# Optimization experiments

Measured on AMD Instinct MI355X. Metric: run time of the kernel, lower is better.

## Reference

```python
import jax, jax.numpy as jnp
import numpy as np

BETA = 0.25  # init kwarg; exercises the 0 <= beta < 1 loss branch


def setup_inputs() -> dict:
    key = jax.random.key(0)
    k1, k2 = jax.random.split(key)
    N, D, K = 65536, 64, 4096
    x = jax.random.normal(k1, (N, D), dtype=jnp.float32)
    # original: uniform(-1/K, 1/K) then mean-centered; exact init distribution
    codebook = jax.random.uniform(k2, (K, D), dtype=jnp.float32,
                                  minval=-1.0 / K, maxval=1.0 / K)
    codebook = codebook - codebook.mean(axis=0, keepdims=True)
    return {"x": x, "codebook": codebook}


def reference(x, codebook):
    # pairwise squared distances via sum-of-squares + matmul: [N, K]
    dist = (jnp.sum(x * x, axis=1, keepdims=True)
            + jnp.sum(codebook * codebook, axis=1)
            - 2.0 * jnp.matmul(x, codebook.T))
    encoding_inds = jnp.argmin(dist, axis=1)            # [N]
    # gather codebook rows (equivalent to one-hot @ codebook, no one-hot materialized)
    quantized = jnp.take(codebook, encoding_inds, axis=0)  # [N, D]
    # straight-through estimator
    x_quantized = x + jax.lax.stop_gradient(quantized - x)
    mse = lambda a, b: jnp.mean((a - b) ** 2)
    loss = (BETA * mse(x, jax.lax.stop_gradient(quantized))
            + mse(quantized, jax.lax.stop_gradient(x)))
    return x_quantized, encoding_inds[:, None], loss
```

## Files before the change

kernel.cpp:

```cpp
#include <hip/hip_runtime.h>


#define D  64
#define NT 256
#define PH 128

typedef unsigned short u16;
typedef short bf16x8 __attribute__((ext_vector_type(8)));
typedef float f32x4  __attribute__((ext_vector_type(4)));

#define VMWAIT(n) asm volatile("s_waitcnt vmcnt(" #n ")" ::: "memory")

__device__ __forceinline__ u16 f32_to_bf16_raw(float f) {
    union { float f; unsigned u; } v; v.f = f;
    unsigned u = v.u;
    u += 0x7FFFu + ((u >> 16) & 1u);
    return (u16)(u >> 16);
}
__device__ __forceinline__ float bf16_raw_to_f32(u16 h) {
    union { unsigned u; float f; } v; v.u = ((unsigned)h) << 16;
    return v.f;
}
__device__ __forceinline__ f32x4 mfma16(bf16x8 a, bf16x8 b, f32x4 c) {
    return __builtin_amdgcn_mfma_f32_16x16x32_bf16(a, b, c, 0, 0, 0);
}

__device__ __forceinline__ float np_pairwise_sumsq_64(const float* p) {
    float r[8];
    #pragma unroll
    for (int j = 0; j < 8; ++j) r[j] = __fmul_rn(p[j], p[j]);
    #pragma unroll
    for (int i = 8; i < 64; i += 8) {
        #pragma unroll
        for (int j = 0; j < 8; ++j)
            r[j] = __fadd_rn(r[j], __fmul_rn(p[i + j], p[i + j]));
    }
    float t0 = __fadd_rn(r[0], r[1]);
    float t1 = __fadd_rn(r[2], r[3]);
    float t2 = __fadd_rn(r[4], r[5]);
    float t3 = __fadd_rn(r[6], r[7]);
    return __fadd_rn(__fadd_rn(t0, t1), __fadd_rn(t2, t3));
}

__global__ __launch_bounds__(256) void rowsumsq_kernel(const float* __restrict__ a,
                                                       float* __restrict__ out, int nrows) {
    int r = blockIdx.x * 256 + threadIdx.x;
    if (r >= nrows) return;
    float buf[64];
    const float4* p = (const float4*)(a + (size_t)r * D);
    #pragma unroll
    for (int i = 0; i < 16; ++i) {
        float4 v = p[i];
        buf[4*i] = v.x; buf[4*i+1] = v.y; buf[4*i+2] = v.z; buf[4*i+3] = v.w;
    }
    out[r] = np_pairwise_sumsq_64(buf);
}

__global__ __launch_bounds__(256) void pack_cb2(const float* __restrict__ cb,
                                                bf16x8* __restrict__ cbf) {
    int t = blockIdx.x;
    int tid = threadIdx.x;
    int lane = tid & 63;
    int ks = (tid >> 6) & 1;
    int hl = tid >> 7;
    int code = t * 16 + (lane & 15);
    int g = lane >> 4;
    bf16x8 v;
    #pragma unroll
    for (int j = 0; j < 8; ++j) {
        int d = ks * 32 + g * 4 + (j & 3) + 16 * (j >> 2);
        float val = cb[(size_t)code * D + d];
        u16 h = f32_to_bf16_raw(val);
        if (hl) {
            float resid = val - bf16_raw_to_f32(h);
            h = f32_to_bf16_raw(resid);
        }
        v[j] = (short)h;
    }
    cbf[((size_t)t * 4 + hl * 2 + ks) * 64 + lane] = v;
}

#define MARG_A 8.0e-6f
#define MARG_B 5.0e-7f

__global__ __launch_bounds__(256, 2) void phase1_kernel(
    const float* __restrict__ x, const float* __restrict__ sx,
    const float* __restrict__ sc, const bf16x8* __restrict__ cbf,
    int* __restrict__ idxbuf, int* __restrict__ amb_cnt, int* __restrict__ amb_rows)
{
    __shared__ __align__(16) char ring[4][8192];
    __shared__ float scl[4096];

    const int tid  = threadIdx.x;
    const int w    = tid >> 6;
    const int lane = tid & 63;
    const int r = lane & 15, g = lane >> 4;
    const int rowA = blockIdx.x * 128 + w * 32 + r;
    const int rowB = rowA + 16;

    for (int j = tid; j < 1024; j += 256)
        *(float4*)&scl[j * 4] = *(const float4*)&sc[j * 4];

    bf16x8 A0h, A1h, A0l, A1l, B0h, B1h, B0l, B1l;
    {
        const float* xr = x + (size_t)rowA * D;
        float e0[8], e1[8];
        float4 f0 = *(const float4*)(xr + g * 4);
        float4 f1 = *(const float4*)(xr + 16 + g * 4);
        float4 f2 = *(const float4*)(xr + 32 + g * 4);
        float4 f3 = *(const float4*)(xr + 48 + g * 4);
        e0[0]=f0.x;e0[1]=f0.y;e0[2]=f0.z;e0[3]=f0.w; e0[4]=f1.x;e0[5]=f1.y;e0[6]=f1.z;e0[7]=f1.w;
        e1[0]=f2.x;e1[1]=f2.y;e1[2]=f2.z;e1[3]=f2.w; e1[4]=f3.x;e1[5]=f3.y;e1[6]=f3.z;e1[7]=f3.w;
        #pragma unroll
        for (int j = 0; j < 8; ++j) {
            u16 h0 = f32_to_bf16_raw(e0[j]);
            A0h[j] = (short)h0; A0l[j] = (short)f32_to_bf16_raw(e0[j] - bf16_raw_to_f32(h0));
            u16 h1 = f32_to_bf16_raw(e1[j]);
            A1h[j] = (short)h1; A1l[j] = (short)f32_to_bf16_raw(e1[j] - bf16_raw_to_f32(h1));
        }
    }
    {
        const float* xr = x + (size_t)rowB * D;
        float e0[8], e1[8];
        float4 f0 = *(const float4*)(xr + g * 4);
        float4 f1 = *(const float4*)(xr + 16 + g * 4);
        float4 f2 = *(const float4*)(xr + 32 + g * 4);
        float4 f3 = *(const float4*)(xr + 48 + g * 4);
        e0[0]=f0.x;e0[1]=f0.y;e0[2]=f0.z;e0[3]=f0.w; e0[4]=f1.x;e0[5]=f1.y;e0[6]=f1.z;e0[7]=f1.w;
        e1[0]=f2.x;e1[1]=f2.y;e1[2]=f2.z;e1[3]=f2.w; e1[4]=f3.x;e1[5]=f3.y;e1[6]=f3.z;e1[7]=f3.w;
        #pragma unroll
        for (int j = 0; j < 8; ++j) {
            u16 h0 = f32_to_bf16_raw(e0[j]);
            B0h[j] = (short)h0; B0l[j] = (short)f32_to_bf16_raw(e0[j] - bf16_raw_to_f32(h0));
            u16 h1 = f32_to_bf16_raw(e1[j]);
            B1h[j] = (short)h1; B1l[j] = (short)f32_to_bf16_raw(e1[j] - bf16_raw_to_f32(h1));
        }
    }

    float sxr[8], m1[8], m2[8];
    int   i1[8];
    #pragma unroll
    for (int u = 0; u < 8; ++u) {
        int orow = blockIdx.x * 128 + w * 32 + (u >> 2) * 16 + g * 4 + (u & 3);
        sxr[u] = sx[orow];
        m1[u] = 3.4e38f; m2[u] = 3.4e38f; i1[u] = 0;
    }

    auto stage = [&](int p, int buf) {
        const char* src = (const char*)cbf + (size_t)p * 8192 + tid * 16;
        #pragma unroll
        for (int i = 0; i < 2; ++i) {
            __builtin_amdgcn_global_load_lds(
                (const __attribute__((address_space(1))) unsigned int*)(src + i * 4096),
                (__attribute__((address_space(3))) unsigned int*)&ring[buf][i * 4096 + w * 1024 + lane * 16],
                16, 0, 0);
        }
    };

    auto compute = [&](int p, int buf) {
        #pragma unroll
        for (int tt = 0; tt < 2; ++tt) {
            int t = 2 * p + tt;
            const bf16x8* bf = (const bf16x8*)&ring[buf][tt * 4096];
            bf16x8 b0h = bf[0 * 64 + lane];
            bf16x8 b1h = bf[1 * 64 + lane];
            bf16x8 b0l = bf[2 * 64 + lane];
            bf16x8 b1l = bf[3 * 64 + lane];

            f32x4 accA = {0.f, 0.f, 0.f, 0.f};
            f32x4 accB = {0.f, 0.f, 0.f, 0.f};
            accA = mfma16(A0h, b0h, accA);  accB = mfma16(B0h, b0h, accB);
            accA = mfma16(A1h, b1h, accA);  accB = mfma16(B1h, b1h, accB);
            accA = mfma16(A0h, b0l, accA);  accB = mfma16(B0h, b0l, accB);
            accA = mfma16(A1h, b1l, accA);  accB = mfma16(B1h, b1l, accB);
            accA = mfma16(A0l, b0h, accA);  accB = mfma16(B0l, b0h, accB);
            accA = mfma16(A1l, b1h, accA);  accB = mfma16(B1l, b1h, accB);

            float sck = scl[t * 16 + r];
            int   kc  = t * 16 + r;
            #pragma unroll
            for (int q = 0; q < 4; ++q) {
                float s = __fmaf_rn(-2.0f, accA[q], __fadd_rn(sxr[q], sck));
                m2[q] = fminf(m2[q], fmaxf(m1[q], s));
                bool lt = s < m1[q];
                i1[q] = lt ? kc : i1[q];
                m1[q] = fminf(m1[q], s);
            }
            #pragma unroll
            for (int q = 0; q < 4; ++q) {
                float s = __fmaf_rn(-2.0f, accB[q], __fadd_rn(sxr[4 + q], sck));
                m2[4+q] = fminf(m2[4+q], fmaxf(m1[4+q], s));
                bool lt = s < m1[4+q];
                i1[4+q] = lt ? kc : i1[4+q];
                m1[4+q] = fminf(m1[4+q], s);
            }
        }
    };

    VMWAIT(0);
    stage(0, 0); stage(1, 1); stage(2, 2);

    for (int p = 0; p < PH - 3; ++p) {
        VMWAIT(4);
        __syncthreads();
        stage(p + 3, (p + 3) & 3);
        compute(p, p & 3);
    }
    VMWAIT(4); __syncthreads(); compute(PH - 3, (PH - 3) & 3);
    VMWAIT(2); __syncthreads(); compute(PH - 2, (PH - 2) & 3);
    VMWAIT(0); __syncthreads(); compute(PH - 1, (PH - 1) & 3);

    #pragma unroll
    for (int u = 0; u < 8; ++u) {
        #pragma unroll
        for (int mm = 1; mm < 16; mm <<= 1) {
            float om1 = __shfl_xor(m1[u], mm, 64);
            float om2 = __shfl_xor(m2[u], mm, 64);
            int   oi1 = __shfl_xor(i1[u], mm, 64);
            float nm2 = fminf(fmaxf(m1[u], om1), fminf(m2[u], om2));
            i1[u] = (om1 < m1[u]) ? oi1 : i1[u];
            m1[u] = fminf(m1[u], om1);
            m2[u] = nm2;
        }
    }
    if (r == 0) {
        #pragma unroll
        for (int u = 0; u < 8; ++u) {
            int orow = blockIdx.x * 128 + w * 32 + (u >> 2) * 16 + g * 4 + (u & 3);
            idxbuf[orow] = i1[u];
            float marg = __fmaf_rn(sxr[u], MARG_B, MARG_A);
            if (m2[u] - m1[u] <= marg) {
                int slot = atomicAdd(amb_cnt, 1);
                amb_rows[slot] = orow;
            }
        }
    }
}

__global__ __launch_bounds__(256) void exact_scan(
    const float* __restrict__ x, const float* __restrict__ cb,
    const float* __restrict__ sx, const float* __restrict__ sc,
    const int* __restrict__ amb_cnt, const int* __restrict__ amb_rows,
    int* __restrict__ idxbuf)
{
    __shared__ float csT[4][64][64];
    __shared__ float xsT[64][16];
    __shared__ float redv[16][64];
    __shared__ int   redi[16][64];
    __shared__ float sxl[16];
    __shared__ int   rowids[16];

    const int tid = threadIdx.x;
    const int cnt = *amb_cnt;
    const int tz = tid >> 6, ty = (tid >> 4) & 3, cx = tid & 15;

    for (int base = blockIdx.x * 16; base < cnt; base += gridDim.x * 16) {
        if (tid < 16) {
            int i = base + tid;
            int rr = (i < cnt) ? amb_rows[i] : amb_rows[base];
            rowids[tid] = rr;
            sxl[tid] = sx[rr];
        }
        __syncthreads();
        {
            int rr = rowids[tid >> 4];
            int dg = tid & 15;
            float4 v = *(const float4*)(x + (size_t)rr * D + dg * 4);
            xsT[dg*4+0][tid>>4] = v.x; xsT[dg*4+1][tid>>4] = v.y;
            xsT[dg*4+2][tid>>4] = v.z; xsT[dg*4+3][tid>>4] = v.w;
        }

        float bv[4]; int bi[4];
        #pragma unroll
        for (int i = 0; i < 4; ++i) { bv[i] = 3.4e38f; bi[i] = 0x7fffffff; }

        for (int st = 0; st < 16; ++st) {
            __syncthreads();
            {
                int code = st * 256 + tid;
                const float4* src = (const float4*)(cb + (size_t)code * D);
                #pragma unroll
                for (int dd = 0; dd < 16; ++dd) {
                    float4 v = src[dd];
                    csT[tid>>6][dd*4+0][tid&63] = v.x; csT[tid>>6][dd*4+1][tid&63] = v.y;
                    csT[tid>>6][dd*4+2][tid&63] = v.z; csT[tid>>6][dd*4+3][tid&63] = v.w;
                }
            }
            __syncthreads();

            float acc[4][4];
            #pragma unroll
            for (int i = 0; i < 4; ++i)
                #pragma unroll
                for (int j = 0; j < 4; ++j) acc[i][j] = 0.0f;

            #pragma unroll 4
            for (int d = 0; d < 64; ++d) {
                float4 xv = *(const float4*)&xsT[d][ty * 4];
                float4 cv = *(const float4*)&csT[tz][d][cx * 4];
                float xr[4] = {xv.x, xv.y, xv.z, xv.w};
                float cc[4] = {cv.x, cv.y, cv.z, cv.w};
                #pragma unroll
                for (int i = 0; i < 4; ++i)
                    #pragma unroll
                    for (int j = 0; j < 4; ++j)
                        acc[i][j] = __fmaf_rn(xr[i], cc[j], acc[i][j]);
            }
            #pragma unroll
            for (int j = 0; j < 4; ++j) {
                int k = st * 256 + tz * 64 + cx * 4 + j;
                float sck = sc[k];
                #pragma unroll
                for (int i = 0; i < 4; ++i) {
                    float tt = __fadd_rn(sxl[ty * 4 + i], sck);
                    float u  = __fmul_rn(2.0f, acc[i][j]);
                    float s  = __fsub_rn(tt, u);
                    if (s < bv[i] || (s == bv[i] && k < bi[i])) { bv[i] = s; bi[i] = k; }
                }
            }
        }

        #pragma unroll
        for (int i = 0; i < 4; ++i) { redv[ty*4+i][tz*16+cx] = bv[i]; redi[ty*4+i][tz*16+cx] = bi[i]; }
        __syncthreads();
        if (tid < 16) {
            float bvv = redv[tid][0]; int bii = redi[tid][0];
            #pragma unroll 8
            for (int i = 1; i < 64; ++i) {
                float v = redv[tid][i]; int k = redi[tid][i];
                if (v < bvv || (v == bvv && k < bii)) { bvv = v; bii = k; }
            }
            idxbuf[rowids[tid]] = bii;
        }
        __syncthreads();
    }
}

__global__ __launch_bounds__(256) void finalize_rows(
    const float* __restrict__ x, const float* __restrict__ cb,
    const int* __restrict__ idxbuf,
    float* __restrict__ out_q, float* __restrict__ out_i,
    double* __restrict__ partials, int N)
{
    __shared__ double wsum[4];
    int wid = threadIdx.x >> 6, lane = threadIdx.x & 63;
    int n = blockIdx.x * 4 + wid;

    int idx = idxbuf[n];
    float q  = cb[(size_t)idx * D + lane];
    float xv = x[(size_t)n * D + lane];
    out_q[(size_t)n * D + lane] = q;

    double diff = (double)xv - (double)q;
    double s = diff * diff;
    #pragma unroll
    for (int off = 32; off > 0; off >>= 1) s += __shfl_down(s, off, 64);
    if (lane == 0) { wsum[wid] = s; out_i[n] = (float)idx; }
    __syncthreads();
    if (threadIdx.x == 0) partials[blockIdx.x] = (wsum[0] + wsum[1]) + (wsum[2] + wsum[3]);
}

__global__ __launch_bounds__(256) void loss_kernel(const double* __restrict__ partials,
                                                   int nP, float* __restrict__ out_loss,
                                                   double invND)
{
    __shared__ double red[256];
    double s = 0.0;
    for (int i = threadIdx.x; i < nP; i += 256) s += partials[i];
    red[threadIdx.x] = s;
    __syncthreads();
    #pragma unroll
    for (int step = 128; step > 0; step >>= 1) {
        if ((int)threadIdx.x < step) red[threadIdx.x] += red[threadIdx.x + step];
        __syncthreads();
    }
    if (threadIdx.x == 0) {
        double m = red[0] * invND;
        out_loss[0] = (float)(0.25 * m + m);
    }
}

extern "C" void kernel_launch(void* const* d_in, const int* in_sizes, int n_in,
                              void* d_out, int out_size, void* d_ws, size_t ws_size,
                              hipStream_t stream)
{
    const float* x  = (const float*)d_in[0];
    const float* cb = (const float*)d_in[1];
    const int N = in_sizes[0] / D;
    const int K = in_sizes[1] / D;

    float* out      = (float*)d_out;
    float* out_q    = out;
    float* out_i    = out + (size_t)N * D;
    float* out_loss = out_i + N;

    char* ws = (char*)d_ws;
    bf16x8* cbf      = (bf16x8*)ws;
    size_t off = (size_t)(K / 16) * 4 * 64 * sizeof(bf16x8);
    float*  sx       = (float*)(ws + off);  off += (size_t)N * 4;
    float*  sc       = (float*)(ws + off);  off += (size_t)K * 4;
    int*    idxbuf   = (int*)(ws + off);    off += (size_t)N * 4;
    int*    amb_rows = (int*)(ws + off);    off += (size_t)N * 4;
    double* partials = (double*)(ws + off); off += (size_t)(N / 4) * 8;
    int*    amb_cnt  = (int*)(ws + off);

    hipMemsetAsync(amb_cnt, 0, sizeof(int), stream);
    rowsumsq_kernel<<<(N + 255) / 256, 256, 0, stream>>>(x, sx, N);
    rowsumsq_kernel<<<(K + 255) / 256, 256, 0, stream>>>(cb, sc, K);
    pack_cb2<<<K / 16, 256, 0, stream>>>(cb, cbf);
    phase1_kernel<<<N / 128, 256, 0, stream>>>(x, sx, sc, cbf, idxbuf, amb_cnt, amb_rows);
    exact_scan<<<512, 256, 0, stream>>>(x, cb, sx, sc, amb_cnt, amb_rows, idxbuf);
    finalize_rows<<<N / 4, 256, 0, stream>>>(x, cb, idxbuf, out_q, out_i, partials, N);
    loss_kernel<<<1, 256, 0, stream>>>(partials, N / 4, out_loss,
                                       1.0 / ((double)N * (double)D));
}
```

Measured before the change: 303.1 us.

## Split codebook across wave pairs with per-wave rings and fuse prep kernels

Merges the memset, both row sum-of-squares kernels and the codebook packing into one prep kernel to cut launch overhead. In phase1 each wave now owns 64 rows and half of the codebook tiles, which doubles A-fragment reuse per loaded B tile and halves the LDS traffic per MFMA. Each wave also streams through its own 3-deep LDS ring without block-wide barriers, using setprio around the MFMA burst. The two halves' top-2 results are merged through shared memory at the end; in exchange register pressure rises (16 rows of state plus 4x A fragments), which could lower occupancy.

```diff
diff --git a/kernel.cpp b/kernel.cpp
--- a/kernel.cpp
+++ b/kernel.cpp
@@ -3,7 +3,6 @@
 
 #define D  64
 #define NT 256
-#define PH 128
 
 typedef unsigned short u16;
 typedef short bf16x8 __attribute__((ext_vector_type(8)));
@@ -42,42 +41,49 @@
     return __fadd_rn(__fadd_rn(t0, t1), __fadd_rn(t2, t3));
 }
 
-__global__ __launch_bounds__(256) void rowsumsq_kernel(const float* __restrict__ a,
-                                                       float* __restrict__ out, int nrows) {
-    int r = blockIdx.x * 256 + threadIdx.x;
-    if (r >= nrows) return;
-    float buf[64];
-    const float4* p = (const float4*)(a + (size_t)r * D);
-    #pragma unroll
-    for (int i = 0; i < 16; ++i) {
-        float4 v = p[i];
-        buf[4*i] = v.x; buf[4*i+1] = v.y; buf[4*i+2] = v.z; buf[4*i+3] = v.w;
-    }
-    out[r] = np_pairwise_sumsq_64(buf);
-}
-
-__global__ __launch_bounds__(256) void pack_cb2(const float* __restrict__ cb,
-                                                bf16x8* __restrict__ cbf) {
-    int t = blockIdx.x;
-    int tid = threadIdx.x;
-    int lane = tid & 63;
-    int ks = (tid >> 6) & 1;
-    int hl = tid >> 7;
-    int code = t * 16 + (lane & 15);
-    int g = lane >> 4;
-    bf16x8 v;
-    #pragma unroll
-    for (int j = 0; j < 8; ++j) {
-        int d = ks * 32 + g * 4 + (j & 3) + 16 * (j >> 2);
-        float val = cb[(size_t)code * D + d];
-        u16 h = f32_to_bf16_raw(val);
-        if (hl) {
-            float resid = val - bf16_raw_to_f32(h);
-            h = f32_to_bf16_raw(resid);
-        }
-        v[j] = (short)h;
-    }
-    cbf[((size_t)t * 4 + hl * 2 + ks) * 64 + lane] = v;
+__global__ __launch_bounds__(256) void prep_kernel(const float* __restrict__ x,
+                                                   const float* __restrict__ cb,
+                                                   float* __restrict__ sx,
+                                                   float* __restrict__ sc,
+                                                   bf16x8* __restrict__ cbf,
+                                                   int* __restrict__ amb_cnt) {
+    int b = blockIdx.x;
+    if (b == 0 && threadIdx.x == 0) *amb_cnt = 0;
+    if (b < 272) {
+        const float* a = (b < 256) ? x : cb;
+        float* o = (b < 256) ? sx : sc;
+        int r0 = (b < 256) ? b * 256 : (b - 256) * 256;
+        int r = r0 + threadIdx.x;
+        float buf[64];
+        const float4* p = (const float4*)(a + (size_t)r * D);
+        #pragma unroll
+        for (int i = 0; i < 16; ++i) {
+            float4 v = p[i];
+            buf[4*i] = v.x; buf[4*i+1] = v.y; buf[4*i+2] = v.z; buf[4*i+3] = v.w;
+        }
+        o[r] = np_pairwise_sumsq_64(buf);
+    } else {
+        int t = b - 272;
+        int tid = threadIdx.x;
+        int lane = tid & 63;
+        int ks = (tid >> 6) & 1;
+        int hl = tid >> 7;
+        int code = t * 16 + (lane & 15);
+        int g = lane >> 4;
+        bf16x8 v;
+        #pragma unroll
+        for (int j = 0; j < 8; ++j) {
+            int d = ks * 32 + g * 4 + (j & 3) + 16 * (j >> 2);
+            float val = cb[(size_t)code * D + d];
+            u16 h = f32_to_bf16_raw(val);
+            if (hl) {
+                float resid = val - bf16_raw_to_f32(h);
+                h = f32_to_bf16_raw(resid);
+            }
+            v[j] = (short)h;
+        }
+        cbf[((size_t)t * 4 + hl * 2 + ks) * 64 + lane] = v;
+    }
 }
 
 #define MARG_A 8.0e-6f
@@ -88,22 +94,27 @@
     const float* __restrict__ sc, const bf16x8* __restrict__ cbf,
     int* __restrict__ idxbuf, int* __restrict__ amb_cnt, int* __restrict__ amb_rows)
 {
-    __shared__ __align__(16) char ring[4][8192];
+    __shared__ __align__(16) char ring[4][3][4096];
     __shared__ float scl[4096];
+    __shared__ float lm1[128][2], lm2[128][2];
+    __shared__ int   li1[128][2];
 
     const int tid  = threadIdx.x;
     const int w    = tid >> 6;
     const int lane = tid & 63;
     const int r = lane & 15, g = lane >> 4;
-    const int rowA = blockIdx.x * 128 + w * 32 + r;
-    const int rowB = rowA + 16;
+    const int half = w & 1;
+    const int rowg = w >> 1;
+    const int wbase = blockIdx.x * 128 + rowg * 64;
 
     for (int j = tid; j < 1024; j += 256)
         *(float4*)&scl[j * 4] = *(const float4*)&sc[j * 4];
-
-    bf16x8 A0h, A1h, A0l, A1l, B0h, B1h, B0l, B1l;
-    {
-        const float* xr = x + (size_t)rowA * D;
+    __syncthreads();
+
+    bf16x8 Ah0[4], Ah1[4], Al0[4], Al1[4];
+    #pragma unroll
+    for (int s = 0; s < 4; ++s) {
+        const float* xr = x + (size_t)(wbase + s * 16 + r) * D;
         float e0[8], e1[8];
         float4 f0 = *(const float4*)(xr + g * 4);
         float4 f1 = *(const float4*)(xr + 16 + g * 4);
@@ -114,104 +125,91 @@
         #pragma unroll
         for (int j = 0; j < 8; ++j) {
             u16 h0 = f32_to_bf16_raw(e0[j]);
-            A0h[j] = (short)h0; A0l[j] = (short)f32_to_bf16_raw(e0[j] - bf16_raw_to_f32(h0));
+            Ah0[s][j] = (short)h0;
+            Al0[s][j] = (short)f32_to_bf16_raw(e0[j] - bf16_raw_to_f32(h0));
             u16 h1 = f32_to_bf16_raw(e1[j]);
-            A1h[j] = (short)h1; A1l[j] = (short)f32_to_bf16_raw(e1[j] - bf16_raw_to_f32(h1));
-        }
-    }
-    {
-        const float* xr = x + (size_t)rowB * D;
-        float e0[8], e1[8];
-        float4 f0 = *(const float4*)(xr + g * 4);
-        float4 f1 = *(const float4*)(xr + 16 + g * 4);
-        float4 f2 = *(const float4*)(xr + 32 + g * 4);
-        float4 f3 = *(const float4*)(xr + 48 + g * 4);
-        e0[0]=f0.x;e0[1]=f0.y;e0[2]=f0.z;e0[3]=f0.w; e0[4]=f1.x;e0[5]=f1.y;e0[6]=f1.z;e0[7]=f1.w;
-        e1[0]=f2.x;e1[1]=f2.y;e1[2]=f2.z;e1[3]=f2.w; e1[4]=f3.x;e1[5]=f3.y;e1[6]=f3.z;e1[7]=f3.w;
-        #pragma unroll
-        for (int j = 0; j < 8; ++j) {
-            u16 h0 = f32_to_bf16_raw(e0[j]);
-            B0h[j] = (short)h0; B0l[j] = (short)f32_to_bf16_raw(e0[j] - bf16_raw_to_f32(h0));
-            u16 h1 = f32_to_bf16_raw(e1[j]);
-            B1h[j] = (short)h1; B1l[j] = (short)f32_to_bf16_raw(e1[j] - bf16_raw_to_f32(h1));
-        }
-    }
-
-    float sxr[8], m1[8], m2[8];
-    int   i1[8];
-    #pragma unroll
-    for (int u = 0; u < 8; ++u) {
-        int orow = blockIdx.x * 128 + w * 32 + (u >> 2) * 16 + g * 4 + (u & 3);
-        sxr[u] = sx[orow];
+            Ah1[s][j] = (short)h1;
+            Al1[s][j] = (short)f32_to_bf16_raw(e1[j] - bf16_raw_to_f32(h1));
+        }
+    }
+
+    float sxr[16], m1[16], m2[16];
+    int   i1[16];
+    #pragma unroll
+    for (int u = 0; u < 16; ++u) {
+        sxr[u] = sx[wbase + (u >> 2) * 16 + g * 4 + (u & 3)];
         m1[u] = 3.4e38f; m2[u] = 3.4e38f; i1[u] = 0;
     }
 
-    auto stage = [&](int p, int buf) {
-        const char* src = (const char*)cbf + (size_t)p * 8192 + tid * 16;
-        #pragma unroll
-        for (int i = 0; i < 2; ++i) {
+    const int t0 = half * 128;
+    char* ringbase = &ring[w][0][0];
+
+    auto stage = [&](int t, int buf) {
+        const char* src = (const char*)cbf + (size_t)t * 4096 + lane * 16;
+        char* dst = ringbase + buf * 4096 + lane * 16;
+        #pragma unroll
+        for (int i = 0; i < 4; ++i)
             __builtin_amdgcn_global_load_lds(
-                (const __attribute__((address_space(1))) unsigned int*)(src + i * 4096),
-                (__attribute__((address_space(3))) unsigned int*)&ring[buf][i * 4096 + w * 1024 + lane * 16],
+                (const __attribute__((address_space(1))) unsigned int*)(src + i * 1024),
+                (__attribute__((address_space(3))) unsigned int*)(dst + i * 1024),
                 16, 0, 0);
-        }
     };
 
-    auto compute = [&](int p, int buf) {
-        #pragma unroll
-        for (int tt = 0; tt < 2; ++tt) {
-            int t = 2 * p + tt;
-            const bf16x8* bf = (const bf16x8*)&ring[buf][tt * 4096];
-            bf16x8 b0h = bf[0 * 64 + lane];
-            bf16x8 b1h = bf[1 * 64 + lane];
-            bf16x8 b0l = bf[2 * 64 + lane];
-            bf16x8 b1l = bf[3 * 64 + lane];
-
-            f32x4 accA = {0.f, 0.f, 0.f, 0.f};
-            f32x4 accB = {0.f, 0.f, 0.f, 0.f};
-            accA = mfma16(A0h, b0h, accA);  accB = mfma16(B0h, b0h, accB);
-            accA = mfma16(A1h, b1h, accA);  accB = mfma16(B1h, b1h, accB);
-            accA = mfma16(A0h, b0l, accA);  accB = mfma16(B0h, b0l, accB);
-            accA = mfma16(A1h, b1l, accA);  accB = mfma16(B1h, b1l, accB);
-            accA = mfma16(A0l, b0h, accA);  accB = mfma16(B0l, b0h, accB);
-            accA = mfma16(A1l, b1h, accA);  accB = mfma16(B1l, b1h, accB);
-
-            float sck = scl[t * 16 + r];
-            int   kc  = t * 16 + r;
+    auto compute = [&](int t, int buf) {
+        const bf16x8* bfr = (const bf16x8*)(ringbase + buf * 4096);
+        bf16x8 b0h = bfr[0 * 64 + lane];
+        bf16x8 b1h = bfr[1 * 64 + lane];
+        bf16x8 b0l = bfr[2 * 64 + lane];
+        bf16x8 b1l = bfr[3 * 64 + lane];
+        float sck = scl[t * 16 + r];
+        int   kc  = t * 16 + r;
+
+        f32x4 acc[4];
+        __builtin_amdgcn_s_setprio(1);
+        #pragma unroll
+        for (int s = 0; s < 4; ++s) {
+            f32x4 a = {0.f, 0.f, 0.f, 0.f};
+            a = mfma16(Ah0[s], b0h, a);
+            a = mfma16(Ah1[s], b1h, a);
+            a = mfma16(Ah0[s], b0l, a);
+            a = mfma16(Ah1[s], b1l, a);
+            a = mfma16(Al0[s], b0h, a);
+            a = mfma16(Al1[s], b1h, a);
+            acc[s] = a;
+        }
+        __builtin_amdgcn_s_setprio(0);
+
+        #pragma unroll
+        for (int s = 0; s < 4; ++s) {
             #pragma unroll
             for (int q = 0; q < 4; ++q) {
-                float s = __fmaf_rn(-2.0f, accA[q], __fadd_rn(sxr[q], sck));
-                m2[q] = fminf(m2[q], fmaxf(m1[q], s));
-                bool lt = s < m1[q];
-                i1[q] = lt ? kc : i1[q];
-                m1[q] = fminf(m1[q], s);
-            }
-            #pragma unroll
-            for (int q = 0; q < 4; ++q) {
-                float s = __fmaf_rn(-2.0f, accB[q], __fadd_rn(sxr[4 + q], sck));
-                m2[4+q] = fminf(m2[4+q], fmaxf(m1[4+q], s));
-                bool lt = s < m1[4+q];
-                i1[4+q] = lt ? kc : i1[4+q];
-                m1[4+q] = fminf(m1[4+q], s);
+                int u = s * 4 + q;
+                float sv = __fmaf_rn(-2.0f, acc[s][q], __fadd_rn(sxr[u], sck));
+                m2[u] = fminf(m2[u], fmaxf(m1[u], sv));
+                bool lt = sv < m1[u];
+                i1[u] = lt ? kc : i1[u];
+                m1[u] = fminf(m1[u], sv);
             }
         }
     };
 
     VMWAIT(0);
-    stage(0, 0); stage(1, 1); stage(2, 2);
-
-    for (int p = 0; p < PH - 3; ++p) {
-        VMWAIT(4);
-        __syncthreads();
-        stage(p + 3, (p + 3) & 3);
-        compute(p, p & 3);
-    }
-    VMWAIT(4); __syncthreads(); compute(PH - 3, (PH - 3) & 3);
-    VMWAIT(2); __syncthreads(); compute(PH - 2, (PH - 2) & 3);
-    VMWAIT(0); __syncthreads(); compute(PH - 1, (PH - 1) & 3);
-
-    #pragma unroll
-    for (int u = 0; u < 8; ++u) {
+    stage(t0 + 0, 0); stage(t0 + 1, 1); stage(t0 + 2, 2);
+
+    #pragma unroll 1
+    for (int i = 0; i < 125; ++i) {
+        VMWAIT(8);
+        compute(t0 + i, i % 3);
+        asm volatile("s_waitcnt lgkmcnt(0)" ::: "memory");
+        __builtin_amdgcn_sched_barrier(0);
+        stage(t0 + i + 3, i % 3);
+    }
+    VMWAIT(8); compute(t0 + 125, 125 % 3);
+    VMWAIT(4); compute(t0 + 126, 126 % 3);
+    VMWAIT(0); compute(t0 + 127, 127 % 3);
+
+    #pragma unroll
+    for (int u = 0; u < 16; ++u) {
         #pragma unroll
         for (int mm = 1; mm < 16; mm <<= 1) {
             float om1 = __shfl_xor(m1[u], mm, 64);
@@ -225,14 +223,28 @@
     }
     if (r == 0) {
         #pragma unroll
-        for (int u = 0; u < 8; ++u) {
-            int orow = blockIdx.x * 128 + w * 32 + (u >> 2) * 16 + g * 4 + (u & 3);
-            idxbuf[orow] = i1[u];
-            float marg = __fmaf_rn(sxr[u], MARG_B, MARG_A);
-            if (m2[u] - m1[u] <= marg) {
-                int slot = atomicAdd(amb_cnt, 1);
-                amb_rows[slot] = orow;
-            }
+        for (int u = 0; u < 16; ++u) {
+            int rowin = rowg * 64 + (u >> 2) * 16 + g * 4 + (u & 3);
+            lm1[rowin][half] = m1[u];
+            lm2[rowin][half] = m2[u];
+            li1[rowin][half] = i1[u];
+        }
+    }
+    __syncthreads();
+
+    if (tid < 128) {
+        float a1 = lm1[tid][0], b1 = lm1[tid][1];
+        float a2 = lm2[tid][0], b2 = lm2[tid][1];
+        int   ia = li1[tid][0], ib = li1[tid][1];
+        float m1f = fminf(a1, b1);
+        float m2f = fminf(fmaxf(a1, b1), fminf(a2, b2));
+        int   i1f = (b1 < a1) ? ib : ia;
+        int orow = blockIdx.x * 128 + tid;
+        idxbuf[orow] = i1f;
+        float marg = __fmaf_rn(sx[orow], MARG_B, MARG_A);
+        if (m2f - m1f <= marg) {
+            int slot = atomicAdd(amb_cnt, 1);
+            amb_rows[slot] = orow;
         }
     }
 }
@@ -404,10 +416,7 @@
     double* partials = (double*)(ws + off); off += (size_t)(N / 4) * 8;
     int*    amb_cnt  = (int*)(ws + off);
 
-    hipMemsetAsync(amb_cnt, 0, sizeof(int), stream);
-    rowsumsq_kernel<<<(N + 255) / 256, 256, 0, stream>>>(x, sx, N);
-    rowsumsq_kernel<<<(K + 255) / 256, 256, 0, stream>>>(cb, sc, K);
-    pack_cb2<<<K / 16, 256, 0, stream>>>(cb, cbf);
+    prep_kernel<<<272 + K / 16, 256, 0, stream>>>(x, cb, sx, sc, cbf, amb_cnt);
     phase1_kernel<<<N / 128, 256, 0, stream>>>(x, sx, sc, cbf, idxbuf, amb_cnt, amb_rows);
     exact_scan<<<512, 256, 0, stream>>>(x, cb, sx, sc, amb_cnt, amb_rows, idxbuf);
     finalize_rows<<<N / 4, 256, 0, stream>>>(x, cb, idxbuf, out_q, out_i, partials, N);
```

Measured after the change: 265.3 us. 1.14x faster.
